# Performance work log

Hardware: AMD Instinct MI355X
Metric: run time of the kernel (lower is better)

## Reference

```python
import jax, jax.numpy as jnp
import numpy as np
import math

B, INST, C, HEADS, DH, CTX = 1, 4, 320, 8, 40, 768
FULL, HW = 512, 4096
SCALE = DH ** -0.5
EPS = 1e-5


def _ln(x, g, b):
    m = x.mean(-1, keepdims=True)
    v = ((x - m) ** 2).mean(-1, keepdims=True)
    return (x - m) / jnp.sqrt(v + EPS) * g + b


def _mha(x, ctx, Wq, Wk, Wv, Wo, bo, mask=None):
    # x: [b, n, C]; ctx: [b, m, ctx_dim]; mask: [b, n, m] bool (True = keep)
    b, n, _ = x.shape
    m = ctx.shape[1]
    q = (x @ Wq).reshape(b, n, HEADS, DH)
    k = (ctx @ Wk).reshape(b, m, HEADS, DH)
    v = (ctx @ Wv).reshape(b, m, HEADS, DH)
    sim = jnp.einsum('bihd,bjhd->bhij', q, k) * SCALE
    if mask is not None:
        sim = jnp.where(mask[:, None, :, :], sim, -jnp.finfo(sim.dtype).max)
    attn = jax.nn.softmax(sim, axis=-1)
    out = jnp.einsum('bhij,bjhd->bihd', attn, v).reshape(b, n, HEADS * DH)
    return out @ Wo + bo


def _fourier(x, num_freqs=8, temperature=100.0):
    freqs = temperature ** (jnp.arange(num_freqs, dtype=x.dtype) / num_freqs)
    parts = []
    for i in range(num_freqs):
        parts.append(jnp.sin(freqs[i] * x))
        parts.append(jnp.cos(freqs[i] * x))
    return jax.lax.stop_gradient(jnp.concatenate(parts, axis=-1))  # @torch.no_grad in source


def _resize(x, H, W):
    # torch F.interpolate bilinear, align_corners=False (half-pixel), no antialias
    return jax.image.resize(x, x.shape[:2] + (H, W), method='bilinear', antialias=False)


def setup_inputs() -> dict:
    key = jax.random.key(0)
    ks = jax.random.split(key, 32)
    s = 0.02
    inp = {
        'ca_x': jax.random.normal(ks[0], (B, INST + 1, HW, C), jnp.float32),
        'guidance_mask': jax.random.uniform(ks[1], (B, INST, FULL, FULL), jnp.float32),
        'supplement_mask': jax.random.uniform(ks[2], (B, 1, FULL, FULL), jnp.float32),
        'image_token': jax.random.normal(ks[3], (B, INST + 1, HW, C), jnp.float32),
        'context': jax.random.normal(ks[4], (INST + 1, 77, CTX), jnp.float32),
        'box': jax.random.uniform(ks[5], (B, INST, 8), jnp.float32),
        'img_features': jax.random.normal(ks[6], (B * INST, 257, CTX), jnp.float32),
        'bg_features': jax.random.normal(ks[7], (B, 257, CTX), jnp.float32),
        'sigmoid_values': jax.random.uniform(ks[8], (B, INST, FULL, FULL), jnp.float32),
        'Wq_obj': jax.random.normal(ks[9], (C, C), jnp.float32) * s,
        'Wk_obj': jax.random.normal(ks[10], (CTX, C), jnp.float32) * s,
        'Wv_obj': jax.random.normal(ks[11], (CTX, C), jnp.float32) * s,
        'Wo_obj': jax.random.normal(ks[12], (C, C), jnp.float32) * s,
        'bo_obj': jnp.zeros((C,), jnp.float32),
        'ln_g_obj': jnp.ones((C,), jnp.float32),
        'ln_b_obj': jnp.zeros((C,), jnp.float32),
        'Wq2': jax.random.normal(ks[13], (C, C), jnp.float32) * s,
        'Wk2': jax.random.normal(ks[14], (CTX, C), jnp.float32) * s,
        'Wv2': jax.random.normal(ks[15], (CTX, C), jnp.float32) * s,
        'Wo2': jax.random.normal(ks[16], (C, C), jnp.float32) * s,
        'bo2': jnp.zeros((C,), jnp.float32),
        'ln_g2': jnp.ones((C,), jnp.float32),
        'ln_b2': jnp.zeros((C,), jnp.float32),
        'pn_W1': jax.random.normal(ks[17], (128, 512), jnp.float32) * s,
        'pn_b1': jnp.zeros((512,), jnp.float32),
        'pn_W2': jax.random.normal(ks[18], (512, 512), jnp.float32) * s,
        'pn_b2': jnp.zeros((512,), jnp.float32),
        'pn_W3': jax.random.normal(ks[19], (512, CTX), jnp.float32) * s,
        'pn_b3': jnp.zeros((CTX,), jnp.float32),
        'la_Wq': jax.random.normal(ks[20], (C, C), jnp.float32) * s,
        'la_Wk': jax.random.normal(ks[21], (C, C), jnp.float32) * s,
        'la_Wv': jax.random.normal(ks[22], (C, C), jnp.float32) * s,
        'la_Wo': jax.random.normal(ks[23], (C, C), jnp.float32) * s,
        'la_bo': jnp.zeros((C,), jnp.float32),
        'height': FULL,
        'width': FULL,
    }
    return inp


def reference(ca_x, guidance_mask, supplement_mask, image_token, context, box,
              img_features, bg_features, sigmoid_values,
              Wq_obj, Wk_obj, Wv_obj, Wo_obj, bo_obj, ln_g_obj, ln_b_obj,
              Wq2, Wk2, Wv2, Wo2, bo2, ln_g2, ln_b2,
              pn_W1, pn_b1, pn_W2, pn_b2, pn_W3, pn_b3,
              la_Wq, la_Wk, la_Wv, la_Wo, la_bo,
              height, width):
    b, _, hw, c = ca_x.shape
    inst = guidance_mask.shape[1]
    down = int(math.sqrt(height * width // hw))
    H, W = height // down, width // down

    gm = _resize(guidance_mask, H, W)           # [B, inst, H, W]
    supp = _resize(supplement_mask, H, W)       # [B, 1, H, W]
    sig = _resize(sigmoid_values, H, W).reshape(b, inst, hw, 1)

    # PositionNet on boxes
    box_emb = _fourier(box.reshape(b * inst, 1, 8))          # [B*inst, 1, 128]
    h1 = jax.nn.silu(box_emb @ pn_W1 + pn_b1)
    h2 = jax.nn.silu(h1 @ pn_W2 + pn_b2)
    box_token = h2 @ pn_W3 + pn_b3                            # [B*inst, 1, 768]

    # foreground cross-attention (ea_obj)
    context_fg = jnp.concatenate([context[1:], img_features, box_token], axis=1)
    q_in = _ln(image_token[:, 1:].reshape(b * inst, hw, c), ln_g_obj, ln_b_obj)
    ea_x = _mha(q_in, context_fg, Wq_obj, Wk_obj, Wv_obj, Wo_obj, bo_obj)
    ea_x = ea_x.reshape(b, inst, hw, c) * sig

    ca_inst = ca_x[:, 1:] * sig + ea_x                        # [B, inst, HW, C]

    # background cross-attention (ea2)
    context_bg = jnp.concatenate([context[0:1], bg_features], axis=1)
    q2 = _ln(ca_inst.sum(axis=1).reshape(b, hw, c), ln_g2, ln_b2)
    ea_bg = _mha(q2, context_bg, Wq2, Wk2, Wv2, Wo2, bo2)     # [B, HW, C]
    ca0 = ca_x[:, 0] + ea_bg

    # layout self-attention with guidance-mask sparsity
    gm_all = jnp.concatenate([gm, supp], axis=1).reshape(b, inst + 1, hw)
    # sum over phases of outer products; clamp-to-1 in source only feeds the ==0 test
    sim_mask = jnp.einsum('bpi,bpj->bij', gm_all, gm_all) != 0  # [B, HW, HW] keep-mask
    fusion = _mha(image_token[:, 0], image_token[:, 0],
                  la_Wq, la_Wk, la_Wv, la_Wo, la_bo, mask=sim_mask)

    out = ca0 + ca_inst.sum(axis=1) + fusion                  # [B, HW, C]
    return out
```

## Files before the change

### kernel.cpp

```cpp
#include <hip/hip_runtime.h>
#include <hip/hip_bf16.h>
#include <math.h>

typedef unsigned short bhalf;
typedef unsigned int u32;
typedef unsigned long long u64;
typedef __attribute__((ext_vector_type(8))) short s16x8;
typedef __attribute__((ext_vector_type(4))) float f32x4;

#define SCALE_QK 0.15811388300841898f
#define K2E (SCALE_QK * 1.4426950408889634f)
#define NEG_INF (-3.402823466e38f)

__device__ __forceinline__ float bf2f(bhalf u){
    union { unsigned int i; float f; } v; v.i = ((unsigned int)u) << 16; return v.f;
}
__device__ __forceinline__ bhalf f2bf(float f){
    unsigned int x = __float_as_uint(f);
    unsigned int r = (x + 0x7fffu + ((x >> 16) & 1u)) >> 16;
    return (bhalf)r;
}
__device__ __forceinline__ float fexp2(float x){
    float r; asm("v_exp_f32 %0, %1" : "=v"(r) : "v"(x)); return r;
}
__device__ __forceinline__ u32 cvtpk(float lo, float hi){
    u32 r; asm("v_cvt_pk_bf16_f32 %0, %1, %2" : "=v"(r) : "v"(lo), "v"(hi)); return r;
}

struct WT12 { const float* in[12]; bhalf* out[12]; };

struct PrepArgs {
    const float *itok, *g_obj, *b_obj; bhalf *q_in, *x_la;
    WT12 wt;
    const float *gmask, *smask, *sgv; float *gm_all, *sig;
    const float *box, *W1, *b1, *W2, *b2, *W3, *b3; float* tok;
};

__global__ __launch_bounds__(320) void mega_prep(PrepArgs a){
    __shared__ float smem[64 * 65];
    const int bid = blockIdx.x, tid = threadIdx.x;
    if (bid < 16){
        float* emb = smem; float* h1 = smem + 128; float* h2 = smem + 640;
        const int bb = bid >> 2, sl = bid & 3;
        for (int t = tid; t < 128; t += 320){
            const int i = t >> 4, jj = t & 15, j = jj & 7;
            const float f = powf(100.f, (float)i * 0.125f);
            const float v = f * a.box[bb * 8 + j];
            emb[t] = (jj < 8) ? sinf(v) : cosf(v);
        }
        __syncthreads();
        for (int t = tid; t < 512; t += 320){
            float a0 = a.b1[t], a1 = 0.f, a2 = 0.f, a3 = 0.f;
#pragma unroll 8
            for (int k = 0; k < 32; ++k){
                a0 += emb[k]      * a.W1[k * 512 + t];
                a1 += emb[k + 32] * a.W1[(k + 32) * 512 + t];
                a2 += emb[k + 64] * a.W1[(k + 64) * 512 + t];
                a3 += emb[k + 96] * a.W1[(k + 96) * 512 + t];
            }
            const float x = (a0 + a1) + (a2 + a3);
            h1[t] = x / (1.f + __expf(-x));
        }
        __syncthreads();
        for (int t = tid; t < 512; t += 320){
            float a0 = a.b2[t], a1 = 0.f, a2 = 0.f, a3 = 0.f;
#pragma unroll 8
            for (int k = 0; k < 128; ++k){
                a0 += h1[k]       * a.W2[k * 512 + t];
                a1 += h1[k + 128] * a.W2[(k + 128) * 512 + t];
                a2 += h1[k + 256] * a.W2[(k + 256) * 512 + t];
                a3 += h1[k + 384] * a.W2[(k + 384) * 512 + t];
            }
            const float x = (a0 + a1) + (a2 + a3);
            h2[t] = x / (1.f + __expf(-x));
        }
        __syncthreads();
        if (tid < 192){
            const int t = sl * 192 + tid;
            float a0 = a.b3[t], a1 = 0.f, a2 = 0.f, a3 = 0.f;
#pragma unroll 8
            for (int k = 0; k < 128; ++k){
                a0 += h2[k]       * a.W3[k * 768 + t];
                a1 += h2[k + 128] * a.W3[(k + 128) * 768 + t];
                a2 += h2[k + 256] * a.W3[(k + 256) * 768 + t];
                a3 += h2[k + 384] * a.W3[(k + 384) * 768 + t];
            }
            a.tok[bb * 768 + t] = (a0 + a1) + (a2 + a3);
        }
    } else if (bid < 456){
        float (*T)[65] = (float(*)[65])smem;
        const int b = bid - 16;
        int w, t, K;
        if (b < 200){ w = b / 25; t = b % 25; K = 320; }
        else        { w = 8 + (b - 200) / 60; t = (b - 200) % 60; K = 768; }
        const int k0 = (t / 5) * 64, n0 = (t % 5) * 64;
        const float* in = a.wt.in[w];
        bhalf* out = a.wt.out[w];
        const int c = tid & 63, wv = tid >> 6;
        if (tid < 256){
#pragma unroll
            for (int r = 0; r < 16; ++r)
                T[wv + r * 4][c] = in[(long)(k0 + wv + r * 4) * 320 + n0 + c];
        }
        __syncthreads();
        if (tid < 256){
#pragma unroll
            for (int r = 0; r < 16; ++r)
                out[(long)(n0 + wv + r * 4) * K + k0 + c] = f2bf(T[c][wv + r * 4]);
        }
    } else if (bid < 600){
        if (tid < 256){
            const int b = bid - 456;
            const int p = b >> 4;
            const int i = (b & 15) * 256 + tid;
            const int y = i >> 6, x = i & 63;
            const int o = (8 * y + 3) * 512 + 8 * x + 3;
            const float* s; float* dst;
            if (p < 4){ s = a.gmask + (long)p * 262144; dst = a.gm_all + p * 4096; }
            else if (p == 4){ s = a.smask; dst = a.gm_all + 4 * 4096; }
            else { s = a.sgv + (long)(p - 5) * 262144; dst = a.sig + (p - 5) * 4096; }
            dst[i] = 0.25f * (s[o] + s[o + 1] + s[o + 512] + s[o + 513]);
        }
    } else {
        const int row = bid - 600, c = tid;
        if (row >= 16384){
            const int rr = row - 16384;
            a.x_la[(long)rr * 320 + c] = f2bf(a.itok[(long)rr * 320 + c]);
            return;
        }
        float* rs = smem; float* rq = smem + 8;
        const float v = a.itok[(long)(4096 + row) * 320 + c];
        float s = v, sq = v * v;
#pragma unroll
        for (int o = 1; o < 64; o <<= 1){ s += __shfl_xor(s, o); sq += __shfl_xor(sq, o); }
        const int wv = tid >> 6;
        if ((tid & 63) == 0){ rs[wv] = s; rq[wv] = sq; }
        __syncthreads();
        if (tid == 0){
            float ts = 0, tq = 0;
#pragma unroll
            for (int w = 0; w < 5; ++w){ ts += rs[w]; tq += rq[w]; }
            rs[0] = ts; rq[0] = tq;
        }
        __syncthreads();
        const float mean = rs[0] * (1.f / 320.f);
        const float var  = rq[0] * (1.f / 320.f) - mean * mean;
        const float inv  = rsqrtf(var + 1e-5f);
        a.q_in[(long)row * 320 + c] = f2bf((v - mean) * inv * a.g_obj[c] + a.b_obj[c]);
    }
}

__global__ __launch_bounds__(256) void mega_mask(
    const float* __restrict__ gm_all, u64* __restrict__ mb,
    const float* __restrict__ context, const float* __restrict__ imgf,
    const float* __restrict__ bgf, const float* __restrict__ boxtok, bhalf* __restrict__ out)
{
    __shared__ float smem[5440];
    const int tid = threadIdx.x;
    if (blockIdx.x < 256){
        const int r = blockIdx.x;
        const int i0 = (r & 63) << 6, j0 = (r >> 6) << 10;
        float* gi = smem;
        float* gj = smem + 320;
        for (int idx = tid; idx < 5 * 64; idx += 256)
            gi[idx] = gm_all[(idx >> 6) * 4096 + i0 + (idx & 63)];
        for (int idx = tid; idx < 5 * 1024; idx += 256)
            gj[idx] = gm_all[(idx >> 10) * 4096 + j0 + (idx & 1023)];
        __syncthreads();
        const int lane = tid & 63, wave = tid >> 6;
        const float a0 = gi[lane], a1 = gi[64 + lane], a2 = gi[128 + lane],
                    a3 = gi[192 + lane], a4 = gi[256 + lane];
        for (int ww = wave; ww < 16; ww += 4){
            u64 m = 0;
            for (int j = 0; j < 64; ++j){
                const int jj = (ww << 6) + j;
                const float dot = a0 * gj[jj] + a1 * gj[1024 + jj] + a2 * gj[2048 + jj]
                                + a3 * gj[3072 + jj] + a4 * gj[4096 + jj];
                m |= (u64)(dot != 0.f) << j;
            }
            mb[(long)((j0 >> 6) + ww) * 4096 + (i0 + lane)] = m;
        }
    } else {
        const int idx = (blockIdx.x - 256) * 256 + tid;
        const int i = idx / (336 * 768);
        const int r = (idx / 768) % 336;
        const int c = idx % 768;
        float v;
        if (i < 4){
            if (r < 77)       v = context[((long)(1 + i) * 77 + r) * 768 + c];
            else if (r < 334) v = imgf[((long)i * 257 + (r - 77)) * 768 + c];
            else if (r == 334) v = boxtok[i * 768 + c];
            else v = 0.f;
        } else {
            if (r < 77)       v = context[(long)r * 768 + c];
            else if (r < 334) v = bgf[(long)(r - 77) * 768 + c];
            else v = 0.f;
        }
        out[idx] = f2bf(v);
    }
}

template<int K>
__device__ __forceinline__ void gemm5_body(
    int bx, int by, const bhalf* __restrict__ A, const bhalf* __restrict__ Wt,
    bhalf* __restrict__ Cbf, int M, int kdm, float scale)
{
    const int wave = threadIdx.x >> 6, lane = threadIdx.x & 63;
    const int m0 = bx * 64 + wave * 16;
    const int n0 = by * 64;
    int mrow = m0 + (lane & 15); if (mrow > M - 1) mrow = M - 1;
    const int klo = (lane >> 4) * 8;
    const bhalf* ap = A + (long)mrow * K + klo;
    const bhalf* wp = Wt + (long)(n0 + (lane & 15)) * K + klo;
    const f32x4 fz = {0.f, 0.f, 0.f, 0.f};
    f32x4 acc[4]; acc[0] = fz; acc[1] = fz; acc[2] = fz; acc[3] = fz;
#pragma unroll
    for (int k0 = 0; k0 < K; k0 += 32){
        s16x8 a = *(const s16x8*)(ap + k0);
#pragma unroll
        for (int t = 0; t < 4; ++t){
            s16x8 b = *(const s16x8*)(wp + (long)t * 16 * K + k0);
            acc[t] = __builtin_amdgcn_mfma_f32_16x16x32_bf16(a, b, acc[t], 0, 0, 0);
        }
    }
    const int rb = m0 + (lane >> 4) * 4;
    int rin[4], rn[4];
#pragma unroll
    for (int r = 0; r < 4; ++r){ const int row = rb + r; rin[r] = row / kdm; rn[r] = row % kdm; }
#pragma unroll
    for (int t = 0; t < 4; ++t){
        const int col = n0 + t * 16 + (lane & 15);
        const int hh = col / 40, cc = col % 40;
#pragma unroll
        for (int r = 0; r < 4; ++r){
            if (rb + r >= M) continue;
            Cbf[(((long)rin[r] * 8 + hh) * kdm + rn[r]) * 40 + cc] = f2bf(acc[t][r] * scale);
        }
    }
}

template<int K>
__device__ __forceinline__ void gemm_vt_body(
    int bx, int by, const bhalf* __restrict__ A, const bhalf* __restrict__ Wt,
    bhalf* __restrict__ Vt, int M, int vt_ns, int PAD, bhalf (*Tsh)[72])
{
    const int wave = threadIdx.x >> 6, lane = threadIdx.x & 63;
    const int m0 = bx * 64 + wave * 16;
    const int n0 = by * 64;
    int mrow = m0 + (lane & 15); if (mrow > M - 1) mrow = M - 1;
    const int klo = (lane >> 4) * 8;
    const bhalf* ap = A + (long)mrow * K + klo;
    const bhalf* wp = Wt + (long)(n0 + (lane & 15)) * K + klo;
    const f32x4 fz = {0.f, 0.f, 0.f, 0.f};
    f32x4 acc[4]; acc[0] = fz; acc[1] = fz; acc[2] = fz; acc[3] = fz;
#pragma unroll
    for (int k0 = 0; k0 < K; k0 += 32){
        s16x8 a = *(const s16x8*)(ap + k0);
#pragma unroll
        for (int t = 0; t < 4; ++t){
            s16x8 b = *(const s16x8*)(wp + (long)t * 16 * K + k0);
            acc[t] = __builtin_amdgcn_mfma_f32_16x16x32_bf16(a, b, acc[t], 0, 0, 0);
        }
    }
    const int hi = lane >> 4, l15 = lane & 15;
#pragma unroll
    for (int t = 0; t < 4; ++t)
#pragma unroll
        for (int r = 0; r < 4; ++r)
            Tsh[wave * 16 + hi * 4 + r][t * 16 + l15] = f2bf(acc[t][r]);
    __syncthreads();
    const int c = threadIdx.x & 63, jq = threadIdx.x >> 6;
    const int jbase = bx * 64 + jq * 16;
    if (jbase >= PAD) return;
    bhalf* vp = Vt + (long)(n0 + c) * vt_ns + jbase;
    if (jbase + 16 <= M){
        u32 wb[8];
#pragma unroll
        for (int p = 0; p < 8; ++p)
            wb[p] = (u32)Tsh[jq * 16 + 2 * p][c] | ((u32)Tsh[jq * 16 + 2 * p + 1][c] << 16);
        *(uint4*)vp       = make_uint4(wb[0], wb[1], wb[2], wb[3]);
        *(uint4*)(vp + 8) = make_uint4(wb[4], wb[5], wb[6], wb[7]);
    } else if (jbase >= M){
        *(uint4*)vp       = make_uint4(0, 0, 0, 0);
        *(uint4*)(vp + 8) = make_uint4(0, 0, 0, 0);
    } else {
        for (int jj = 0; jj < 16; ++jj)
            vp[jj] = (jbase + jj < M) ? Tsh[jq * 16 + jj][c] : (bhalf)0;
    }
}

struct ProjArgs {
    const bhalf *q_in, *ctx_all, *x_la;
    const bhalf *wqobjT, *wkobjT, *wk2T, *lawqT, *wvobjT, *wv2T, *lawvT;
    bhalf *q_obj, *k_obj, *k_bg, *qkl, *vt_obj, *vt_bg, *vt_l;
};

__global__ __launch_bounds__(256) void mega_proj(ProjArgs a){
    __shared__ bhalf Tsh[64][72];
    const int r = blockIdx.x;
    if (r < 1280)      gemm5_body<320>(r % 256, r / 256, a.q_in, a.wqobjT, a.q_obj, 16384, 4096, K2E);
    else if (r < 1385){ const int s = r - 1280; gemm5_body<768>(s % 21, s / 21, a.ctx_all, a.wkobjT, a.k_obj, 1344, 336, 1.f); }
    else if (r < 1415){ const int s = r - 1385; gemm5_body<768>(s % 6, s / 6, a.ctx_all + (size_t)4 * 336 * 768, a.wk2T, a.k_bg, 336, 336, 1.f); }
    else if (r < 2055){ const int s = r - 1415; const int by = s / 64, bx = s % 64;
        gemm5_body<320>(bx, by, a.x_la, a.lawqT, a.qkl, 4096, 4096, by < 5 ? K2E : 1.f); }
    else if (r < 2205){ const int s = r - 2055; const int bz = s / 30, rem = s % 30;
        if (bz == 4) gemm_vt_body<768>(rem % 6, rem / 6, a.ctx_all + (size_t)4 * 336 * 768, a.wv2T, a.vt_bg, 336, 384, 384, Tsh);
        else gemm_vt_body<768>(rem % 6, rem / 6, a.ctx_all + (size_t)bz * 336 * 768, a.wvobjT, a.vt_obj + (size_t)bz * 320 * 384, 336, 384, 384, Tsh);
    }
    else { const int s = r - 2205; gemm_vt_body<320>(s % 64, s / 64, a.x_la, a.lawvT, a.vt_l, 4096, 4096, 4096, Tsh); }
}

__global__ __launch_bounds__(320) void ln_rows_kernel(
    const float* __restrict__ in, const float* __restrict__ g, const float* __restrict__ b,
    bhalf* __restrict__ out)
{
    const int row = blockIdx.x, c = threadIdx.x;
    const float v = in[(long)row * 320 + c];
    float s = v, sq = v * v;
#pragma unroll
    for (int o = 1; o < 64; o <<= 1){ s += __shfl_xor(s, o); sq += __shfl_xor(sq, o); }
    __shared__ float rs[5], rq[5];
    const int wv = threadIdx.x >> 6;
    if ((threadIdx.x & 63) == 0){ rs[wv] = s; rq[wv] = sq; }
    __syncthreads();
    if (threadIdx.x == 0){
        float ts = 0, tq = 0;
#pragma unroll
        for (int w = 0; w < 5; ++w){ ts += rs[w]; tq += rq[w]; }
        rs[0] = ts; rq[0] = tq;
    }
    __syncthreads();
    const float mean = rs[0] * (1.f / 320.f);
    const float var  = rq[0] * (1.f / 320.f) - mean * mean;
    const float inv  = rsqrtf(var + 1e-5f);
    out[(long)row * 320 + c] = f2bf((v - mean) * inv * g[c] + b[c]);
}

template<int MODE>
__global__ __launch_bounds__(256) void gemm320(
    const bhalf* __restrict__ A, const bhalf* __restrict__ Wt,
    const float* __restrict__ bias, bhalf* __restrict__ Cbf,
    float* __restrict__ Cf, const float* __restrict__ add1, const float* __restrict__ add2,
    int M, int kdm, float ascale,
    const bhalf* __restrict__ A2, const bhalf* __restrict__ Wt2, const float* __restrict__ bias2)
{
    constexpr int K = 320;
    const int wave = threadIdx.x >> 6, lane = threadIdx.x & 63;
    const int m0 = blockIdx.x * 64 + wave * 16;
    const int n0 = blockIdx.y * 64;
    int mrow = m0 + (lane & 15); if (mrow > M - 1) mrow = M - 1;
    const int klo = (lane >> 4) * 8;
    const bhalf* ap = A + (long)mrow * K + klo;
    const bhalf* wp = Wt + (long)(n0 + (lane & 15)) * K + klo;
    const f32x4 fz = {0.f, 0.f, 0.f, 0.f};
    f32x4 acc[4]; acc[0] = fz; acc[1] = fz; acc[2] = fz; acc[3] = fz;
#pragma unroll
    for (int k0 = 0; k0 < K; k0 += 32){
        s16x8 a = *(const s16x8*)(ap + k0);
#pragma unroll
        for (int t = 0; t < 4; ++t){
            s16x8 b = *(const s16x8*)(wp + (long)t * 16 * K + k0);
            acc[t] = __builtin_amdgcn_mfma_f32_16x16x32_bf16(a, b, acc[t], 0, 0, 0);
        }
    }
    if (MODE == 6){
        const bhalf* ap2 = A2 + (long)mrow * K + klo;
        const bhalf* wp2 = Wt2 + (long)(n0 + (lane & 15)) * K + klo;
#pragma unroll
        for (int k0 = 0; k0 < K; k0 += 32){
            s16x8 a = *(const s16x8*)(ap2 + k0);
#pragma unroll
            for (int t = 0; t < 4; ++t){
                s16x8 b = *(const s16x8*)(wp2 + (long)t * 16 * K + k0);
                acc[t] = __builtin_amdgcn_mfma_f32_16x16x32_bf16(a, b, acc[t], 0, 0, 0);
            }
        }
    }
    if (MODE == 8){
#pragma unroll
        for (int i = 1; i < 4; ++i){
            const bhalf* api = A + (long)i * kdm + (long)mrow * K + klo;
#pragma unroll
            for (int k0 = 0; k0 < K; k0 += 32){
                s16x8 a = *(const s16x8*)(api + k0);
#pragma unroll
                for (int t = 0; t < 4; ++t){
                    s16x8 b = *(const s16x8*)(wp + (long)t * 16 * K + k0);
                    acc[t] = __builtin_amdgcn_mfma_f32_16x16x32_bf16(a, b, acc[t], 0, 0, 0);
                }
            }
        }
    }
    const int rb = m0 + (lane >> 4) * 4;
    int rin[4], rn[4];
    if (MODE == 5){
#pragma unroll
        for (int r = 0; r < 4; ++r){ const int row = rb + r; rin[r] = row / kdm; rn[r] = row % kdm; }
    }
#pragma unroll
    for (int t = 0; t < 4; ++t){
        const int col = n0 + t * 16 + (lane & 15);
        const int hh = col / 40, cc = col % 40;
#pragma unroll
        for (int r = 0; r < 4; ++r){
            const int row = rb + r;
            if (row >= M) continue;
            const float v = acc[t][r];
            if (MODE == 5)
                Cbf[(((long)rin[r] * 8 + hh) * kdm + rn[r]) * 40 + cc] = f2bf(v * ascale);
            else if (MODE == 6){
                const long o = (long)row * 320 + col;
                Cf[o] = v + bias[col] + bias2[col] + add1[o] + add2[o];
            }
            else if (MODE == 8){
                const long o = (long)row * 320 + col;
                float ssum = 0.f, cax = 0.f;
#pragma unroll
                for (int i = 0; i < 4; ++i){
                    const float sg = add2[i * 4096 + row];
                    ssum += sg;
                    cax += sg * add1[(long)i * 4096 * 320 + o];
                }
                Cf[o] = v + ssum * bias[col] + cax;
            }
        }
    }
}

template<bool GMM, bool PARTIAL, bool SIG>
__global__ __launch_bounds__(256) void flash4(
    const bhalf* __restrict__ Qh, const bhalf* __restrict__ Kh, const bhalf* __restrict__ Vt,
    bhalf* __restrict__ O, const u64* __restrict__ maskb,
    int NKV, long qh_is, long qh_hs, long kh_is, long kh_hs, long vt_is, int vt_ns, long o_is,
    const float* __restrict__ sigp, bhalf* __restrict__ pacc, float* __restrict__ pl)
{
    const int lane = threadIdx.x & 63, wave = threadIdx.x >> 6;
    const int l15 = lane & 15, hi = lane >> 4, klo = hi * 8;
    const int h = blockIdx.y;
    const int inst = PARTIAL ? 0 : blockIdx.z;
    const int g = PARTIAL ? blockIdx.z : 0;
    const int qbase = blockIdx.x * 256 + wave * 64;
    const s16x8 z8 = {0, 0, 0, 0, 0, 0, 0, 0};
    const f32x4 fz = {0.f, 0.f, 0.f, 0.f};

    s16x8 qa0[4], qa1[4];
#pragma unroll
    for (int qg = 0; qg < 4; ++qg){
        const bhalf* qp = Qh + inst * qh_is + h * qh_hs + (long)(qbase + qg * 16 + l15) * 40;
        qa0[qg] = *(const s16x8*)(qp + klo);
        qa1[qg] = (hi == 0) ? *(const s16x8*)(qp + 32) : z8;
    }
    const int krbase = 8 * (l15 >> 2) + (l15 & 3);
    const bhalf* khead = Kh + inst * kh_is + h * kh_hs;
    const bhalf* kbase = khead + (long)krbase * 40;

    const bhalf* vbase[3];
#pragma unroll
    for (int ct = 0; ct < 3; ++ct){
        int dr = h * 40 + ct * 16 + l15; if (dr > 319) dr = 319;
        vbase[ct] = Vt + inst * vt_is + (long)dr * vt_ns + hi * 8;
    }

    f32x4 acc[4][3];
    float l_run[4];
#pragma unroll
    for (int qg = 0; qg < 4; ++qg){
        acc[qg][0] = fz; acc[qg][1] = fz; acc[qg][2] = fz;
        l_run[qg] = 0.f;
    }

    auto soft_pv = [&](f32x4 (&d)[4], s16x8 (&vb)[3][2], float& lr, f32x4 (&ac)[3]){
        float csum = 0.f;
#pragma unroll
        for (int t = 0; t < 4; ++t)
#pragma unroll
            for (int r = 0; r < 4; ++r){
                const float p = fexp2(d[t][r]);
                d[t][r] = p; csum += p;
            }
        csum += __shfl_xor(csum, 16);
        csum += __shfl_xor(csum, 32);
        lr += csum;
#pragma unroll
        for (int s = 0; s < 2; ++s){
            union { u32 w[4]; s16x8 v; } pb;
            pb.w[0] = cvtpk(d[2 * s][0], d[2 * s][1]);
            pb.w[1] = cvtpk(d[2 * s][2], d[2 * s][3]);
            pb.w[2] = cvtpk(d[2 * s + 1][0], d[2 * s + 1][1]);
            pb.w[3] = cvtpk(d[2 * s + 1][2], d[2 * s + 1][3]);
#pragma unroll
            for (int ct = 0; ct < 3; ++ct)
                ac[ct] = __builtin_amdgcn_mfma_f32_16x16x32_bf16(vb[ct][s], pb.v, ac[ct], 0, 0, 0);
        }
    };

    const int ch0 = PARTIAL ? g * 8 : 0;
    const int chN = PARTIAL ? ch0 + 8 : (NKV >> 6);
    for (int ch = ch0; ch < chN; ++ch){
        const int c0 = ch << 6;
        s16x8 k0[4], k1[4];
#pragma unroll
        for (int t = 0; t < 4; ++t){
            const int toff = ((t >> 1) << 5) + ((t & 1) << 2);
            const bhalf* kp = kbase + (long)(c0 + toff) * 40;
            k0[t] = *(const s16x8*)(kp + klo);
            k1[t] = (hi == 0) ? *(const s16x8*)(kp + 32) : z8;
        }
        s16x8 vb[3][2];
#pragma unroll
        for (int ct = 0; ct < 3; ++ct)
#pragma unroll
            for (int s = 0; s < 2; ++s)
                vb[ct][s] = *(const s16x8*)(vbase[ct] + c0 + 32 * s);
        u64 M[4];
        if (GMM){
#pragma unroll
            for (int qg = 0; qg < 4; ++qg)
                M[qg] = maskb[(long)ch * 4096 + qbase + qg * 16 + l15];
        }
#pragma unroll
        for (int qg = 0; qg < 4; ++qg){
            f32x4 d[4];
#pragma unroll
            for (int t = 0; t < 4; ++t){
                d[t] = __builtin_amdgcn_mfma_f32_16x16x32_bf16(k0[t], qa0[qg], fz, 0, 0, 0);
                d[t] = __builtin_amdgcn_mfma_f32_16x16x32_bf16(k1[t], qa1[qg], d[t], 0, 0, 0);
            }
            if (GMM && !__all(M[qg] == ~0ull)){
                const u64 Mh = M[qg] >> (hi * 8);
#pragma unroll
                for (int t = 0; t < 4; ++t){
                    const int tb = ((t >> 1) << 5) + ((t & 1) << 2);
#pragma unroll
                    for (int r = 0; r < 4; ++r)
                        if (!((Mh >> (tb + r)) & 1)) d[t][r] = NEG_INF;
                }
            }
            soft_pv(d, vb, l_run[qg], acc[qg]);
        }
    }
    if (!PARTIAL && (NKV & 63)){
        const int c0 = (NKV >> 6) << 6;
        s16x8 k0[4], k1[4];
#pragma unroll
        for (int t = 0; t < 4; ++t){
            const int toff = ((t >> 1) << 5) + ((t & 1) << 2);
            int kr = c0 + toff + krbase; if (kr > NKV - 1) kr = NKV - 1;
            const bhalf* kp = khead + (long)kr * 40;
            k0[t] = *(const s16x8*)(kp + klo);
            k1[t] = (hi == 0) ? *(const s16x8*)(kp + 32) : z8;
        }
        s16x8 vb[3][2];
#pragma unroll
        for (int ct = 0; ct < 3; ++ct)
#pragma unroll
            for (int s = 0; s < 2; ++s)
                vb[ct][s] = *(const s16x8*)(vbase[ct] + c0 + 32 * s);
#pragma unroll
        for (int qg = 0; qg < 4; ++qg){
            f32x4 d[4];
#pragma unroll
            for (int t = 0; t < 4; ++t){
                d[t] = __builtin_amdgcn_mfma_f32_16x16x32_bf16(k0[t], qa0[qg], fz, 0, 0, 0);
                d[t] = __builtin_amdgcn_mfma_f32_16x16x32_bf16(k1[t], qa1[qg], d[t], 0, 0, 0);
            }
#pragma unroll
            for (int t = 0; t < 4; ++t){
                const int tb = ((t >> 1) << 5) + ((t & 1) << 2);
#pragma unroll
                for (int r = 0; r < 4; ++r)
                    if (c0 + tb + hi * 8 + r >= NKV) d[t][r] = NEG_INF;
            }
            soft_pv(d, vb, l_run[qg], acc[qg]);
        }
    }

    if (PARTIAL){
#pragma unroll
        for (int qg = 0; qg < 4; ++qg){
            const int q = qbase + qg * 16 + l15;
#pragma unroll
            for (int ct = 0; ct < 3; ++ct){
                bhalf* pb = pacc + ((((size_t)(g * 8 + h) * 3 + ct) * 4 + hi) * 4096 + q) * 4;
                uint2 w;
                w.x = cvtpk(acc[qg][ct][0], acc[qg][ct][1]);
                w.y = cvtpk(acc[qg][ct][2], acc[qg][ct][3]);
                *(uint2*)pb = w;
            }
            if (hi == 0)
                pl[(size_t)(g * 8 + h) * 4096 + q] = l_run[qg];
        }
    } else {
#pragma unroll
        for (int qg = 0; qg < 4; ++qg){
            const int q = qbase + qg * 16 + l15;
            float sc = 1.f / l_run[qg];
            if (SIG) sc *= sigp[(long)inst * 4096 + q];
            bhalf* op = O + inst * o_is + (long)q * 320 + h * 40;
#pragma unroll
            for (int ct = 0; ct < 3; ++ct){
                const int d0 = ct * 16 + hi * 4;
                if (d0 < 40){
                    uint2 w;
                    w.x = cvtpk(acc[qg][ct][0] * sc, acc[qg][ct][1] * sc);
                    w.y = cvtpk(acc[qg][ct][2] * sc, acc[qg][ct][3] * sc);
                    *(uint2*)(op + d0) = w;
                }
            }
        }
    }
}

__global__ __launch_bounds__(256) void combine_kernel(
    const bhalf* __restrict__ pacc, const float* __restrict__ pl, bhalf* __restrict__ O)
{
    const int idx = blockIdx.x * 256 + threadIdx.x;
    const int h = idx / (3 * 4096);
    const int r2 = idx % (3 * 4096);
    const int ct = r2 >> 12, q = r2 & 4095;
    float ls = 0.f;
#pragma unroll
    for (int g = 0; g < 8; ++g) ls += pl[(size_t)(g * 8 + h) * 4096 + q];
    float acc[16];
#pragma unroll
    for (int d = 0; d < 16; ++d) acc[d] = 0.f;
#pragma unroll
    for (int g = 0; g < 8; ++g){
#pragma unroll
        for (int hi = 0; hi < 4; ++hi){
            const ushort4 v = *(const ushort4*)(pacc + ((((size_t)(g * 8 + h) * 3 + ct) * 4 + hi) * 4096 + q) * 4);
            acc[hi * 4 + 0] += bf2f(v.x);
            acc[hi * 4 + 1] += bf2f(v.y);
            acc[hi * 4 + 2] += bf2f(v.z);
            acc[hi * 4 + 3] += bf2f(v.w);
        }
    }
    const float inv = 1.f / ls;
    bhalf* op = O + (size_t)q * 320 + h * 40 + ct * 16;
    if (ct < 2){
        u32 wb[8];
#pragma unroll
        for (int d = 0; d < 8; ++d) wb[d] = cvtpk(acc[2 * d] * inv, acc[2 * d + 1] * inv);
        *(uint4*)op       = make_uint4(wb[0], wb[1], wb[2], wb[3]);
        *(uint4*)(op + 8) = make_uint4(wb[4], wb[5], wb[6], wb[7]);
    } else {
        u32 wb[4];
#pragma unroll
        for (int d = 0; d < 4; ++d) wb[d] = cvtpk(acc[2 * d] * inv, acc[2 * d + 1] * inv);
        *(uint4*)op = make_uint4(wb[0], wb[1], wb[2], wb[3]);
    }
}

extern "C" void kernel_launch(void* const* d_in, const int* in_sizes, int n_in,
                              void* d_out, int out_size, void* d_ws, size_t ws_size,
                              hipStream_t stream)
{
    (void)in_sizes; (void)n_in; (void)out_size; (void)ws_size;
    const float* ca_x   = (const float*)d_in[0];
    const float* gmask  = (const float*)d_in[1];
    const float* smask  = (const float*)d_in[2];
    const float* itok   = (const float*)d_in[3];
    const float* ctx    = (const float*)d_in[4];
    const float* box    = (const float*)d_in[5];
    const float* imgf   = (const float*)d_in[6];
    const float* bgf    = (const float*)d_in[7];
    const float* sgv    = (const float*)d_in[8];
    const float* Wq_obj = (const float*)d_in[9];
    const float* Wk_obj = (const float*)d_in[10];
    const float* Wv_obj = (const float*)d_in[11];
    const float* Wo_obj = (const float*)d_in[12];
    const float* bo_obj = (const float*)d_in[13];
    const float* g_obj  = (const float*)d_in[14];
    const float* b_obj  = (const float*)d_in[15];
    const float* Wq2    = (const float*)d_in[16];
    const float* Wk2    = (const float*)d_in[17];
    const float* Wv2    = (const float*)d_in[18];
    const float* Wo2    = (const float*)d_in[19];
    const float* bo2    = (const float*)d_in[20];
    const float* g2     = (const float*)d_in[21];
    const float* b2     = (const float*)d_in[22];
    const float* pnW1   = (const float*)d_in[23];
    const float* pnb1   = (const float*)d_in[24];
    const float* pnW2   = (const float*)d_in[25];
    const float* pnb2   = (const float*)d_in[26];
    const float* pnW3   = (const float*)d_in[27];
    const float* pnb3   = (const float*)d_in[28];
    const float* laWq   = (const float*)d_in[29];
    const float* laWk   = (const float*)d_in[30];
    const float* laWv   = (const float*)d_in[31];
    const float* laWo   = (const float*)d_in[32];
    const float* labo   = (const float*)d_in[33];

    char* wsp = (char*)d_ws; size_t off = 0;
    auto alloc = [&](size_t bytes) -> void* {
        void* p = wsp + off; off += (bytes + 255) & ~(size_t)255; return p;
    };
    bhalf* wqobjT = (bhalf*)alloc(320 * 320 * 2);
    bhalf* woobjT = (bhalf*)alloc(320 * 320 * 2);
    bhalf* wq2T   = (bhalf*)alloc(320 * 320 * 2);
    bhalf* wo2T   = (bhalf*)alloc(320 * 320 * 2);
    bhalf* lawqT  = (bhalf*)alloc(320 * 320 * 2);
    bhalf* lawkT  = (bhalf*)alloc(320 * 320 * 2);
    bhalf* lawvT  = (bhalf*)alloc(320 * 320 * 2);
    bhalf* lawoT  = (bhalf*)alloc(320 * 320 * 2);
    bhalf* wkobjT = (bhalf*)alloc(768 * 320 * 2);
    bhalf* wvobjT = (bhalf*)alloc(768 * 320 * 2);
    bhalf* wk2T   = (bhalf*)alloc(768 * 320 * 2);
    bhalf* wv2T   = (bhalf*)alloc(768 * 320 * 2);
    float* gm_all = (float*)alloc(5 * 4096 * 4);
    float* sig    = (float*)alloc(4 * 4096 * 4);
    float* boxtok = (float*)alloc(4 * 768 * 4);
    u64*   maskb  = (u64*)alloc((size_t)64 * 4096 * 8);
    bhalf* ctx_all= (bhalf*)alloc((size_t)5 * 336 * 768 * 2);
    bhalf* q_in   = (bhalf*)alloc((size_t)16384 * 320 * 2);
    bhalf* x_la   = (bhalf*)alloc((size_t)4096 * 320 * 2);
    bhalf* k_obj  = (bhalf*)alloc((size_t)4 * 336 * 320 * 2);
    bhalf* vt_obj = (bhalf*)alloc((size_t)4 * 320 * 384 * 2);
    bhalf* k_bg   = (bhalf*)alloc((size_t)336 * 320 * 2);
    bhalf* vt_bg  = (bhalf*)alloc((size_t)320 * 384 * 2);
    bhalf* q_obj  = (bhalf*)alloc((size_t)16384 * 320 * 2);
    bhalf* o_obj  = (bhalf*)alloc((size_t)16384 * 320 * 2);
    float* Sbuf   = (float*)alloc((size_t)4096 * 320 * 4);
    bhalf* q2v    = (bhalf*)alloc((size_t)4096 * 320 * 2);
    bhalf* q2p    = (bhalf*)alloc((size_t)4096 * 320 * 2);
    bhalf* o2     = (bhalf*)alloc((size_t)4096 * 320 * 2);
    bhalf* qkl    = (bhalf*)alloc((size_t)2 * 4096 * 320 * 2);
    bhalf* vt_l   = (bhalf*)alloc((size_t)320 * 4096 * 2);
    bhalf* ol     = (bhalf*)alloc((size_t)4096 * 320 * 2);

    bhalf* pacc = (bhalf*)q_in;
    float* pl   = (float*)(pacc + (size_t)8 * 8 * 3 * 4 * 4096 * 4);

    PrepArgs pa{};
    pa.itok = itok; pa.g_obj = g_obj; pa.b_obj = b_obj; pa.q_in = q_in; pa.x_la = x_la;
    pa.wt.in[0] = Wq_obj; pa.wt.out[0] = wqobjT;
    pa.wt.in[1] = Wo_obj; pa.wt.out[1] = woobjT;
    pa.wt.in[2] = Wq2;    pa.wt.out[2] = wq2T;
    pa.wt.in[3] = Wo2;    pa.wt.out[3] = wo2T;
    pa.wt.in[4] = laWq;   pa.wt.out[4] = lawqT;
    pa.wt.in[5] = laWk;   pa.wt.out[5] = lawkT;
    pa.wt.in[6] = laWv;   pa.wt.out[6] = lawvT;
    pa.wt.in[7] = laWo;   pa.wt.out[7] = lawoT;
    pa.wt.in[8] = Wk_obj; pa.wt.out[8] = wkobjT;
    pa.wt.in[9] = Wv_obj; pa.wt.out[9] = wvobjT;
    pa.wt.in[10] = Wk2;   pa.wt.out[10] = wk2T;
    pa.wt.in[11] = Wv2;   pa.wt.out[11] = wv2T;
    pa.gmask = gmask; pa.smask = smask; pa.sgv = sgv; pa.gm_all = gm_all; pa.sig = sig;
    pa.box = box; pa.W1 = pnW1; pa.b1 = pnb1; pa.W2 = pnW2; pa.b2 = pnb2; pa.W3 = pnW3; pa.b3 = pnb3;
    pa.tok = boxtok;
    mega_prep<<<dim3(21080), 320, 0, stream>>>(pa);

    mega_mask<<<dim3(5296), 256, 0, stream>>>(gm_all, maskb, ctx, imgf, bgf, boxtok, ctx_all);

    ProjArgs pj{};
    pj.q_in = q_in; pj.ctx_all = ctx_all; pj.x_la = x_la;
    pj.wqobjT = wqobjT; pj.wkobjT = wkobjT; pj.wk2T = wk2T; pj.lawqT = lawqT;
    pj.wvobjT = wvobjT; pj.wv2T = wv2T; pj.lawvT = lawvT;
    pj.q_obj = q_obj; pj.k_obj = k_obj; pj.k_bg = k_bg; pj.qkl = qkl;
    pj.vt_obj = vt_obj; pj.vt_bg = vt_bg; pj.vt_l = vt_l;
    mega_proj<<<dim3(2525), 256, 0, stream>>>(pj);

    flash4<false, false, true><<<dim3(16, 8, 4), 256, 0, stream>>>(q_obj, k_obj, vt_obj, o_obj, nullptr,
        335, (long)8 * 4096 * 40, (long)4096 * 40, (long)8 * 336 * 40, (long)336 * 40,
        (long)320 * 384, 384, (long)4096 * 320, sig, nullptr, nullptr);

    gemm320<8><<<dim3(64, 5), 256, 0, stream>>>(o_obj, woobjT, bo_obj, nullptr, Sbuf,
        ca_x + (size_t)4096 * 320, sig, 4096, 4096 * 320, 1.f, nullptr, nullptr, nullptr);

    ln_rows_kernel<<<dim3(4096), 320, 0, stream>>>(Sbuf, g2, b2, q2v);

    gemm320<5><<<dim3(64, 5), 256, 0, stream>>>(q2v, wq2T, nullptr, q2p, nullptr, nullptr, nullptr,
        4096, 4096, K2E, nullptr, nullptr, nullptr);

    flash4<false, false, false><<<dim3(16, 8, 1), 256, 0, stream>>>(q2p, k_bg, vt_bg, o2, nullptr,
        334, 0, (long)4096 * 40, 0, (long)336 * 40, 0, 384, 0, nullptr, nullptr, nullptr);

    flash4<true, true, false><<<dim3(16, 8, 8), 256, 0, stream>>>(qkl, qkl + (size_t)8 * 4096 * 40, vt_l, nullptr, maskb,
        4096, 0, (long)4096 * 40, 0, (long)4096 * 40, 0, 4096, 0, nullptr, pacc, pl);

    combine_kernel<<<dim3(384), 256, 0, stream>>>(pacc, pl, ol);

    gemm320<6><<<dim3(64, 5), 256, 0, stream>>>(o2, wo2T, bo2, nullptr, (float*)d_out, ca_x, Sbuf,
        4096, 1, 1.f, ol, lawoT, labo);
}
```

Measured before the change: 313.3 us.

## Use 64-row-per-wave projection tiles, split proj launch, wave-per-row layernorm

The Q/K projection GEMM body now computes a 64x64 tile per wave (4x4 MFMA fragments) instead of 16x64, which reuses each loaded B fragment across four A fragments and cuts the block count. The mega projection launch is split into a packed-GEMM kernel and a separate V-transpose kernel. Layernorm rows in both the prep kernel and ln_rows_kernel are now handled one per wave using a shuffle-only reduction, which removes the shared-memory barriers and shrinks the grids. In exchange, the larger tiles raise register pressure and leave fewer blocks to spread across the GPU, and the extra launch adds a dependency point.

```diff
diff --git a/kernel.cpp b/kernel.cpp
--- a/kernel.cpp
+++ b/kernel.cpp
@@ -122,31 +122,36 @@
             dst[i] = 0.25f * (s[o] + s[o + 1] + s[o + 512] + s[o + 513]);
         }
     } else {
-        const int row = bid - 600, c = tid;
-        if (row >= 16384){
-            const int rr = row - 16384;
-            a.x_la[(long)rr * 320 + c] = f2bf(a.itok[(long)rr * 320 + c]);
-            return;
-        }
-        float* rs = smem; float* rq = smem + 8;
-        const float v = a.itok[(long)(4096 + row) * 320 + c];
-        float s = v, sq = v * v;
-#pragma unroll
-        for (int o = 1; o < 64; o <<= 1){ s += __shfl_xor(s, o); sq += __shfl_xor(sq, o); }
-        const int wv = tid >> 6;
-        if ((tid & 63) == 0){ rs[wv] = s; rq[wv] = sq; }
-        __syncthreads();
-        if (tid == 0){
-            float ts = 0, tq = 0;
-#pragma unroll
-            for (int w = 0; w < 5; ++w){ ts += rs[w]; tq += rq[w]; }
-            rs[0] = ts; rq[0] = tq;
-        }
-        __syncthreads();
-        const float mean = rs[0] * (1.f / 320.f);
-        const float var  = rq[0] * (1.f / 320.f) - mean * mean;
-        const float inv  = rsqrtf(var + 1e-5f);
-        a.q_in[(long)row * 320 + c] = f2bf((v - mean) * inv * a.g_obj[c] + a.b_obj[c]);
+        const int lane = tid & 63, wv = tid >> 6;
+        const int wgid = (bid - 600) * 5 + wv;
+        for (int row = wgid; row < 20480; row += 10240){
+            if (row >= 16384){
+                const int rr = row - 16384;
+#pragma unroll
+                for (int j = 0; j < 5; ++j){
+                    const int c = lane + 64 * j;
+                    a.x_la[(long)rr * 320 + c] = f2bf(a.itok[(long)rr * 320 + c]);
+                }
+                continue;
+            }
+            float v[5];
+            float s = 0.f, sq = 0.f;
+#pragma unroll
+            for (int j = 0; j < 5; ++j){
+                v[j] = a.itok[(long)(4096 + row) * 320 + lane + 64 * j];
+                s += v[j]; sq += v[j] * v[j];
+            }
+#pragma unroll
+            for (int o = 1; o < 64; o <<= 1){ s += __shfl_xor(s, o); sq += __shfl_xor(sq, o); }
+            const float mean = s * (1.f / 320.f);
+            const float var  = sq * (1.f / 320.f) - mean * mean;
+            const float inv  = rsqrtf(var + 1e-5f);
+#pragma unroll
+            for (int j = 0; j < 5; ++j){
+                const int c = lane + 64 * j;
+                a.q_in[(long)row * 320 + c] = f2bf((v[j] - mean) * inv * a.g_obj[c] + a.b_obj[c]);
+            }
+        }
     }
 }
 
@@ -201,40 +206,54 @@
 }
 
 template<int K>
-__device__ __forceinline__ void gemm5_body(
+__device__ __forceinline__ void gemm5x4_body(
     int bx, int by, const bhalf* __restrict__ A, const bhalf* __restrict__ Wt,
     bhalf* __restrict__ Cbf, int M, int kdm, float scale)
 {
     const int wave = threadIdx.x >> 6, lane = threadIdx.x & 63;
-    const int m0 = bx * 64 + wave * 16;
+    const int mb = bx * 256 + wave * 64;
     const int n0 = by * 64;
-    int mrow = m0 + (lane & 15); if (mrow > M - 1) mrow = M - 1;
     const int klo = (lane >> 4) * 8;
-    const bhalf* ap = A + (long)mrow * K + klo;
+    const bhalf* ap[4];
+#pragma unroll
+    for (int f = 0; f < 4; ++f){
+        int mrow = mb + f * 16 + (lane & 15); if (mrow > M - 1) mrow = M - 1;
+        ap[f] = A + (long)mrow * K + klo;
+    }
     const bhalf* wp = Wt + (long)(n0 + (lane & 15)) * K + klo;
     const f32x4 fz = {0.f, 0.f, 0.f, 0.f};
-    f32x4 acc[4]; acc[0] = fz; acc[1] = fz; acc[2] = fz; acc[3] = fz;
+    f32x4 acc[4][4];
+#pragma unroll
+    for (int f = 0; f < 4; ++f)
+#pragma unroll
+        for (int t = 0; t < 4; ++t) acc[f][t] = fz;
 #pragma unroll
     for (int k0 = 0; k0 < K; k0 += 32){
-        s16x8 a = *(const s16x8*)(ap + k0);
+        s16x8 av[4];
+#pragma unroll
+        for (int f = 0; f < 4; ++f) av[f] = *(const s16x8*)(ap[f] + k0);
+        s16x8 bv[4];
+#pragma unroll
+        for (int t = 0; t < 4; ++t) bv[t] = *(const s16x8*)(wp + (long)t * 16 * K + k0);
+#pragma unroll
+        for (int f = 0; f < 4; ++f)
+#pragma unroll
+            for (int t = 0; t < 4; ++t)
+                acc[f][t] = __builtin_amdgcn_mfma_f32_16x16x32_bf16(av[f], bv[t], acc[f][t], 0, 0, 0);
+    }
+#pragma unroll
+    for (int f = 0; f < 4; ++f){
+        const int rb = mb + f * 16 + ((threadIdx.x & 63) >> 4) * 4;
 #pragma unroll
         for (int t = 0; t < 4; ++t){
-            s16x8 b = *(const s16x8*)(wp + (long)t * 16 * K + k0);
-            acc[t] = __builtin_amdgcn_mfma_f32_16x16x32_bf16(a, b, acc[t], 0, 0, 0);
-        }
-    }
-    const int rb = m0 + (lane >> 4) * 4;
-    int rin[4], rn[4];
-#pragma unroll
-    for (int r = 0; r < 4; ++r){ const int row = rb + r; rin[r] = row / kdm; rn[r] = row % kdm; }
-#pragma unroll
-    for (int t = 0; t < 4; ++t){
-        const int col = n0 + t * 16 + (lane & 15);
-        const int hh = col / 40, cc = col % 40;
-#pragma unroll
-        for (int r = 0; r < 4; ++r){
-            if (rb + r >= M) continue;
-            Cbf[(((long)rin[r] * 8 + hh) * kdm + rn[r]) * 40 + cc] = f2bf(acc[t][r] * scale);
+            const int col = n0 + t * 16 + (threadIdx.x & 15);
+            const int hh = col / 40, cc = col % 40;
+#pragma unroll
+            for (int r = 0; r < 4; ++r){
+                const int row = rb + r;
+                if (row >= M) continue;
+                Cbf[(((long)(row / kdm) * 8 + hh) * kdm + (row % kdm)) * 40 + cc] = f2bf(acc[f][t][r] * scale);
+            }
         }
     }
 }
@@ -295,45 +314,50 @@
     bhalf *q_obj, *k_obj, *k_bg, *qkl, *vt_obj, *vt_bg, *vt_l;
 };
 
-__global__ __launch_bounds__(256) void mega_proj(ProjArgs a){
+__global__ __launch_bounds__(256) void proj_packed(ProjArgs a){
+    const int r = blockIdx.x;
+    if (r < 320)       gemm5x4_body<320>(r % 64, r / 64, a.q_in, a.wqobjT, a.q_obj, 16384, 4096, K2E);
+    else if (r < 480){ const int s = r - 320; const int by = s / 16, bx = s % 16;
+        gemm5x4_body<320>(bx, by, a.x_la, a.lawqT, a.qkl, 4096, 4096, by < 5 ? K2E : 1.f); }
+    else if (r < 510){ const int s = r - 480; gemm5x4_body<768>(s % 6, s / 6, a.ctx_all, a.wkobjT, a.k_obj, 1344, 336, 1.f); }
+    else { const int s = r - 510; gemm5x4_body<768>(s % 2, s / 2, a.ctx_all + (size_t)4 * 336 * 768, a.wk2T, a.k_bg, 336, 336, 1.f); }
+}
+
+__global__ __launch_bounds__(256) void proj_vt(ProjArgs a){
     __shared__ bhalf Tsh[64][72];
     const int r = blockIdx.x;
-    if (r < 1280)      gemm5_body<320>(r % 256, r / 256, a.q_in, a.wqobjT, a.q_obj, 16384, 4096, K2E);
-    else if (r < 1385){ const int s = r - 1280; gemm5_body<768>(s % 21, s / 21, a.ctx_all, a.wkobjT, a.k_obj, 1344, 336, 1.f); }
-    else if (r < 1415){ const int s = r - 1385; gemm5_body<768>(s % 6, s / 6, a.ctx_all + (size_t)4 * 336 * 768, a.wk2T, a.k_bg, 336, 336, 1.f); }
-    else if (r < 2055){ const int s = r - 1415; const int by = s / 64, bx = s % 64;
-        gemm5_body<320>(bx, by, a.x_la, a.lawqT, a.qkl, 4096, 4096, by < 5 ? K2E : 1.f); }
-    else if (r < 2205){ const int s = r - 2055; const int bz = s / 30, rem = s % 30;
+    if (r < 150){ const int bz = r / 30, rem = r % 30;
         if (bz == 4) gemm_vt_body<768>(rem % 6, rem / 6, a.ctx_all + (size_t)4 * 336 * 768, a.wv2T, a.vt_bg, 336, 384, 384, Tsh);
         else gemm_vt_body<768>(rem % 6, rem / 6, a.ctx_all + (size_t)bz * 336 * 768, a.wvobjT, a.vt_obj + (size_t)bz * 320 * 384, 336, 384, 384, Tsh);
     }
-    else { const int s = r - 2205; gemm_vt_body<320>(s % 64, s / 64, a.x_la, a.lawvT, a.vt_l, 4096, 4096, 4096, Tsh); }
-}
-
-__global__ __launch_bounds__(320) void ln_rows_kernel(
+    else { const int s = r - 150; gemm_vt_body<320>(s % 64, s / 64, a.x_la, a.lawvT, a.vt_l, 4096, 4096, 4096, Tsh); }
+}
+
+__global__ __launch_bounds__(256) void ln_rows_kernel(
     const float* __restrict__ in, const float* __restrict__ g, const float* __restrict__ b,
     bhalf* __restrict__ out)
 {
-    const int row = blockIdx.x, c = threadIdx.x;
-    const float v = in[(long)row * 320 + c];
-    float s = v, sq = v * v;
-#pragma unroll
-    for (int o = 1; o < 64; o <<= 1){ s += __shfl_xor(s, o); sq += __shfl_xor(sq, o); }
-    __shared__ float rs[5], rq[5];
-    const int wv = threadIdx.x >> 6;
-    if ((threadIdx.x & 63) == 0){ rs[wv] = s; rq[wv] = sq; }
-    __syncthreads();
-    if (threadIdx.x == 0){
-        float ts = 0, tq = 0;
-#pragma unroll
-        for (int w = 0; w < 5; ++w){ ts += rs[w]; tq += rq[w]; }
-        rs[0] = ts; rq[0] = tq;
-    }
-    __syncthreads();
-    const float mean = rs[0] * (1.f / 320.f);
-    const float var  = rq[0] * (1.f / 320.f) - mean * mean;
-    const float inv  = rsqrtf(var + 1e-5f);
-    out[(long)row * 320 + c] = f2bf((v - mean) * inv * g[c] + b[c]);
+    const int lane = threadIdx.x & 63;
+    const int wgid = blockIdx.x * 4 + (threadIdx.x >> 6);
+    for (int row = wgid; row < 4096; row += 4096){
+        float v[5];
+        float s = 0.f, sq = 0.f;
+#pragma unroll
+        for (int j = 0; j < 5; ++j){
+            v[j] = in[(long)row * 320 + lane + 64 * j];
+            s += v[j]; sq += v[j] * v[j];
+        }
+#pragma unroll
+        for (int o = 1; o < 64; o <<= 1){ s += __shfl_xor(s, o); sq += __shfl_xor(sq, o); }
+        const float mean = s * (1.f / 320.f);
+        const float var  = sq * (1.f / 320.f) - mean * mean;
+        const float inv  = rsqrtf(var + 1e-5f);
+#pragma unroll
+        for (int j = 0; j < 5; ++j){
+            const int c = lane + 64 * j;
+            out[(long)row * 320 + c] = f2bf((v[j] - mean) * inv * g[c] + b[c]);
+        }
+    }
 }
 
 template<int MODE>
@@ -748,7 +772,7 @@
     pa.gmask = gmask; pa.smask = smask; pa.sgv = sgv; pa.gm_all = gm_all; pa.sig = sig;
     pa.box = box; pa.W1 = pnW1; pa.b1 = pnb1; pa.W2 = pnW2; pa.b2 = pnb2; pa.W3 = pnW3; pa.b3 = pnb3;
     pa.tok = boxtok;
-    mega_prep<<<dim3(21080), 320, 0, stream>>>(pa);
+    mega_prep<<<dim3(2648), 320, 0, stream>>>(pa);
 
     mega_mask<<<dim3(5296), 256, 0, stream>>>(gm_all, maskb, ctx, imgf, bgf, boxtok, ctx_all);
 
@@ -758,7 +782,8 @@
     pj.wvobjT = wvobjT; pj.wv2T = wv2T; pj.lawvT = lawvT;
     pj.q_obj = q_obj; pj.k_obj = k_obj; pj.k_bg = k_bg; pj.qkl = qkl;
     pj.vt_obj = vt_obj; pj.vt_bg = vt_bg; pj.vt_l = vt_l;
-    mega_proj<<<dim3(2525), 256, 0, stream>>>(pj);
+    proj_packed<<<dim3(520), 256, 0, stream>>>(pj);
+    proj_vt<<<dim3(470), 256, 0, stream>>>(pj);
 
     flash4<false, false, true><<<dim3(16, 8, 4), 256, 0, stream>>>(q_obj, k_obj, vt_obj, o_obj, nullptr,
         335, (long)8 * 4096 * 40, (long)4096 * 40, (long)8 * 336 * 40, (long)336 * 40,
@@ -767,7 +792,7 @@
     gemm320<8><<<dim3(64, 5), 256, 0, stream>>>(o_obj, woobjT, bo_obj, nullptr, Sbuf,
         ca_x + (size_t)4096 * 320, sig, 4096, 4096 * 320, 1.f, nullptr, nullptr, nullptr);
 
-    ln_rows_kernel<<<dim3(4096), 320, 0, stream>>>(Sbuf, g2, b2, q2v);
+    ln_rows_kernel<<<dim3(1024), 256, 0, stream>>>(Sbuf, g2, b2, q2v);
 
     gemm320<5><<<dim3(64, 5), 256, 0, stream>>>(q2v, wq2T, nullptr, q2p, nullptr, nullptr, nullptr,
         4096, 4096, K2E, nullptr, nullptr, nullptr);
```

Measured after the change: 321.6 us. 1.03x slower.
